# Performance work log

Measured on AMD Instinct MI355X. Metric: run time of the kernel, lower is better.

## Reference

```python
import jax, jax.numpy as jnp
import numpy as np
from jax.scipy.linalg import solve_triangular


def setup_inputs() -> dict:
    key = jax.random.key(0)
    k1, k2 = jax.random.split(key)
    # [K classes, N per class, D features] training embeddings
    src_seq = jax.random.normal(k1, (256, 64, 128), dtype=jnp.float32)
    # [M, D] vectors to project and pairwise-score (clustering inner loop)
    test = jax.random.normal(k2, (8192, 128), dtype=jnp.float32)
    return {"src_seq": src_seq, "test": test}


def _fit_model(src_seq):
    # Faithful port of compute_scatter_matrices + fit_model.
    # S_w, S_b are symmetric PSD, so solve(S_w,S_b) eig is replaced by the
    # equivalent (and differentiable) generalized symmetric eig via Cholesky
    # whitening; A_inverse and psi are invariant to eigvec scaling/order.
    K, N, D = src_seq.shape
    count = K * N
    mean_per_class = src_seq.mean(axis=1)            # [K, D]
    mean = src_seq.mean(axis=(0, 1))                 # [D]
    diff_w = src_seq - mean_per_class[:, None, :]    # [K, N, D]
    diff_b = mean_per_class - mean                   # [K, D]
    S_w = jnp.einsum('knd,kne->de', diff_w, diff_w) / count   # [D, D]
    S_b = (N * jnp.einsum('kd,ke->de', diff_b, diff_b)) / count

    L = jnp.linalg.cholesky(S_w)                     # S_w = L L^T
    # Msym = L^{-1} S_b L^{-T}
    tmp = solve_triangular(L, S_b, lower=True)
    Msym = solve_triangular(L, tmp.T, lower=True).T
    Msym = 0.5 * (Msym + Msym.T)
    evals, U = jnp.linalg.eigh(Msym)
    W = solve_triangular(L, U, lower=True, trans=1)  # W = L^{-T} U, eigvecs of S_w^{-1} S_b

    lambda_b = jnp.sum(W * (S_b @ W), axis=0)        # diag(W^T S_b W)
    lambda_w = jnp.sum(W * (S_w @ W), axis=0)        # diag(W^T S_w W)
    n = float(N)
    # A = W^{-T} diag(sqrt(n/(n-1) * lambda_w))  =>  A^{-1} = diag(1/sqrt(.)) W^T
    A_inverse = (1.0 / jnp.sqrt(n / (n - 1.0) * lambda_w))[:, None] * W.T
    psi = jnp.clip((n - 1.0) / n * (lambda_b / lambda_w) - 1.0 / n, 0.0)
    return A_inverse, mean, psi


def reference(src_seq, test):
    A_inverse, mean, psi = _fit_model(src_seq)
    # latent = A_inverse @ (x - mean), batched over rows
    latent = (test - mean) @ A_inverse.T             # [M, D]
    # Pairwise single-vector probability (calculate_probability_single),
    # vectorized over all (i, j) pairs, in log space:
    # log p(i,j) = -(v_i - v_j)^T diag(psi) (v_i - v_j)
    #             - 0.5 * (D*log(2*pi) + log(||psi||_F))
    D = latent.shape[1]
    q = jnp.sum(psi * latent * latent, axis=1)       # [M]
    G = (latent * psi) @ latent.T                    # [M, M]
    maha = q[:, None] + q[None, :] - 2.0 * G         # [M, M]
    log_div = 0.5 * (D * jnp.log(2.0 * jnp.pi) + jnp.log(jnp.linalg.norm(psi)))
    return -maha - log_div                           # [M, M] pairwise log-prob
```

## Files before the change

### kernel.cpp

```cpp
#include <hip/hip_runtime.h>
#include <math.h>


#define D 128
#define NCLS 256
#define NPC 64
#define MTEST 8192
#define COUNT (NCLS*NPC)

#define fMC    0
#define fMEAN  16384
#define fSCAL  16640
#define fMAT   32768
#define fSWRAW 442368
#define fPART  458752
#define fU     458752
#define fV     983040
#define fQ     1507328
#define fBBF   1515520

#define sP   0
#define sSB  1
#define sP2  2
#define sP3  3
#define sP4  4
#define sZ   5
#define sMm  7
#define sC2  8
#define sXH  10
#define sT2  11
#define sT3  12
#define sT4  13
#define sT8  14
#define sT12 15
#define sT16 16
#define sG0  18
#define sF   23

using short8 = __attribute__((ext_vector_type(8))) short;
using f32x4  = __attribute__((ext_vector_type(4))) float;

__device__ inline unsigned short f2bf(float f) {
  unsigned u = __float_as_uint(f);
  unsigned r = u + 0x7FFFu + ((u >> 16) & 1u);
  return (unsigned short)(r >> 16);
}
__device__ inline float bf2f(unsigned short h) {
  return __uint_as_float(((unsigned)h) << 16);
}
__device__ inline float valU(const unsigned short* m, int idx) {
  return bf2f(m[idx]) + bf2f(m[idx + 16384]);
}
__device__ inline void storeDual(unsigned short* m, int idx, float g) {
  unsigned short hb = f2bf(g);
  m[idx] = hb;
  m[16384 + idx] = f2bf(g - bf2f(hb));
}
__device__ inline unsigned short* MS(float* ws, int m) {
  return (unsigned short*)(ws + fMAT) + (size_t)m * 32768;
}
__device__ inline short8 st8(const unsigned short* L, int rloc, int colk) {
  unsigned u = ((unsigned)(rloc * 128 + colk)) ^ (((unsigned)(rloc & 7)) << 3);
  return *(const short8*)(L + u);
}
__device__ inline float stValU(const unsigned short* L, int rloc, int col) {
  unsigned u = ((unsigned)(rloc * 128 + col)) ^ (((unsigned)(rloc & 7)) << 3);
  return bf2f(L[u]) + bf2f(L[4096 + u]);
}
__device__ inline void stPutDual(unsigned short* L, int rloc, int col, float g) {
  unsigned u = ((unsigned)(rloc * 128 + col)) ^ (((unsigned)(rloc & 7)) << 3);
  unsigned short hb = f2bf(g);
  L[u] = hb;
  L[4096 + u] = f2bf(g - bf2f(hb));
}

__device__ __forceinline__ f32x4 tile_AB(const unsigned short* __restrict__ A, int rA,
                                         const unsigned short* __restrict__ B, int cB,
                                         int lane, f32x4 acc) {
  #pragma unroll
  for (int ks = 0; ks < 4; ks++) {
    int kb = ks * 32 + (lane >> 4) * 8;
    short8 ah = *(const short8*)(A + rA * 128 + kb);
    short8 al = *(const short8*)(A + 16384 + rA * 128 + kb);
    short8 bh = *(const short8*)(B + cB * 128 + kb);
    short8 bl = *(const short8*)(B + 16384 + cB * 128 + kb);
    acc = __builtin_amdgcn_mfma_f32_16x16x32_bf16(ah, bh, acc, 0, 0, 0);
    acc = __builtin_amdgcn_mfma_f32_16x16x32_bf16(al, bh, acc, 0, 0, 0);
    acc = __builtin_amdgcn_mfma_f32_16x16x32_bf16(ah, bl, acc, 0, 0, 0);
  }
  return acc;
}
__device__ __forceinline__ f32x4 tile_LB(const unsigned short* __restrict__ L, int rloc,
                                         const unsigned short* __restrict__ B, int cB,
                                         int lane, f32x4 acc) {
  #pragma unroll
  for (int ks = 0; ks < 4; ks++) {
    int kb = ks * 32 + (lane >> 4) * 8;
    short8 ah = st8(L, rloc, kb);
    short8 al = st8(L + 4096, rloc, kb);
    short8 bh = *(const short8*)(B + cB * 128 + kb);
    short8 bl = *(const short8*)(B + 16384 + cB * 128 + kb);
    acc = __builtin_amdgcn_mfma_f32_16x16x32_bf16(ah, bh, acc, 0, 0, 0);
    acc = __builtin_amdgcn_mfma_f32_16x16x32_bf16(al, bh, acc, 0, 0, 0);
    acc = __builtin_amdgcn_mfma_f32_16x16x32_bf16(ah, bl, acc, 0, 0, 0);
  }
  return acc;
}

__global__ __launch_bounds__(256) void k_gt_partial(const float* __restrict__ X, float* __restrict__ ws) {
  __shared__ unsigned short xt[128 * 256];
  int b = blockIdx.x, tid = threadIdx.x;
  const float* Xc = X + b * 256 * D;
  for (int idx = tid; idx < 256 * D; idx += 256) {
    int s = idx >> 7, d = idx & 127;
    unsigned byte = ((unsigned)(d * 512 + s * 2)) ^ (((unsigned)(d & 7)) << 4);
    *(unsigned short*)((char*)xt + byte) = f2bf(Xc[idx]);
  }
  {
    int d = tid & 127;
    for (int cc = (tid >> 7); cc < 4; cc += 2) {
      const float* p = Xc + cc * 64 * D + d;
      float s = 0.f;
      #pragma unroll
      for (int n = 0; n < 64; n++) s += p[n * D];
      ((unsigned short*)ws)[d * 256 + (b * 4 + cc)] = f2bf(s * (1.0f / 64.0f));
    }
  }
  __syncthreads();
  int w = tid >> 6, lane = tid & 63;
  int wr = (w >> 1) * 64, wc = (w & 1) * 64;
  f32x4 acc[4][4] = {};
  for (int ks = 0; ks < 8; ks++) {
    int kb = ks * 32 + (lane >> 4) * 8;
    short8 af[4];
    #pragma unroll
    for (int mt = 0; mt < 4; mt++) {
      int r = wr + mt * 16 + (lane & 15);
      unsigned byte = ((unsigned)(r * 512 + kb * 2)) ^ (((unsigned)(r & 7)) << 4);
      af[mt] = *(short8*)((char*)xt + byte);
    }
    #pragma unroll
    for (int nt = 0; nt < 4; nt++) {
      int c = wc + nt * 16 + (lane & 15);
      unsigned byte = ((unsigned)(c * 512 + kb * 2)) ^ (((unsigned)(c & 7)) << 4);
      short8 bfr = *(short8*)((char*)xt + byte);
      #pragma unroll
      for (int mt = 0; mt < 4; mt++)
        acc[mt][nt] = __builtin_amdgcn_mfma_f32_16x16x32_bf16(af[mt], bfr, acc[mt][nt], 0, 0, 0);
    }
  }
  float* outp = ws + fPART + b * 16384;
  #pragma unroll
  for (int mt = 0; mt < 4; mt++)
    #pragma unroll
    for (int nt = 0; nt < 4; nt++)
      #pragma unroll
      for (int r = 0; r < 4; r++) {
        int row = wr + mt * 16 + (lane >> 4) * 4 + r;
        int col = wc + nt * 16 + (lane & 15);
        outp[row * 128 + col] = acc[mt][nt][r];
      }
}

__global__ void k_reduce(float* __restrict__ ws) {
  __shared__ float red2[4];
  int tid = threadIdx.x;
  int idx = blockIdx.x * 256 + tid;
  const float* part = ws + fPART;
  float s = 0.f;
  #pragma unroll 8
  for (int p = 0; p < 64; p++) s += part[p * 16384 + idx];
  ws[fSWRAW + idx] = s;
  if (blockIdx.x == 0 && tid < 128) {
    const unsigned short* McT = (const unsigned short*)ws;
    float m = 0.f;
    for (int k = 0; k < 256; k++) m += bf2f(McT[tid * 256 + k]);
    ws[fMEAN + tid] = m * (1.0f / 256.0f);
  }
  if (blockIdx.x == 1) {
    float v = 0.f;
    if (tid < 128) {
      float gdd = 0.f;
      for (int p = 0; p < 64; p++) gdd += part[p * 16384 + tid * 129];
      const unsigned short* McT = (const unsigned short*)ws;
      float nrm = 0.f;
      for (int k = 0; k < 256; k++) { float x = bf2f(McT[tid * 256 + k]); nrm += x * x; }
      v = gdd * (1.0f / COUNT) - nrm * (1.0f / 256.0f);
    }
    #pragma unroll
    for (int off = 32; off > 0; off >>= 1) v += __shfl_down(v, off);
    if ((tid & 63) == 0) red2[tid >> 6] = v;
    __syncthreads();
    if (tid == 0) {
      float inv_s = 128.0f / (red2[0] + red2[1] + red2[2] + red2[3]);
      ws[fSCAL + 1] = inv_s;
      ws[fSCAL + 7] = 0.984375f * inv_s;
    }
  }
}

__global__ __launch_bounds__(1024) void k_sbp(float* __restrict__ ws) {
  const unsigned short* Mc = (const unsigned short*)ws;
  const float* mv = ws + fMEAN;
  const float* swraw = ws + fSWRAW;
  float inv_s = ws[fSCAL + 1];
  unsigned short* SB = MS(ws, sSB);
  unsigned short* P = MS(ws, sP);
  int tid = threadIdx.x, b = blockIdx.x;
  int w = tid >> 6, lane = tid & 63;
  int wr = (w & 1) * 16, wc = (w >> 1) * 16;
  int brow = b * 32;
  f32x4 acc = {};
  for (int ks = 0; ks < 8; ks++) {
    int kb = ks * 32 + (lane >> 4) * 8;
    short8 af = *(const short8*)(Mc + (brow + wr + (lane & 15)) * 256 + kb);
    short8 bf = *(const short8*)(Mc + (wc + (lane & 15)) * 256 + kb);
    acc = __builtin_amdgcn_mfma_f32_16x16x32_bf16(af, bf, acc, 0, 0, 0);
  }
  #pragma unroll
  for (int r = 0; r < 4; r++) {
    int row = brow + wr + (lane >> 4) * 4 + r;
    int col = wc + (lane & 15);
    int idx = row * 128 + col;
    float g = acc[r] * (1.0f / 256.0f) - mv[row] * mv[col];
    storeDual(SB, idx, g);
    float s = (swraw[idx] * (1.0f / COUNT) - g - mv[row] * mv[col]) * inv_s;
    storeDual(P, idx, s - ((row == col) ? 1.0f : 0.0f));
  }
}

__global__ __launch_bounds__(1024) void k_pows(const float* __restrict__ test, float* __restrict__ ws) {
  __shared__ unsigned short sA[8192];
  __shared__ unsigned short sB[8192];
  __shared__ float red[16];
  float* scal = ws + fSCAL;
  int tid = threadIdx.x, b = blockIdx.x;
  if (b >= 4) {
    unsigned short* Vbf = (unsigned short*)(ws + fV);
    const float* mv = ws + fMEAN;
    int base = (b - 4) * 32768;
    #pragma unroll 4
    for (int k = 0; k < 32; k++) {
      int idx = base + k * 1024 + tid;
      Vbf[idx] = f2bf(test[idx] - mv[idx & 127]);
    }
    return;
  }
  const unsigned short* P = MS(ws, sP);
  unsigned short* P2 = MS(ws, sP2);
  unsigned short* P3 = MS(ws, sP3);
  unsigned short* P4 = MS(ws, sP4);
  int w = tid >> 6, lane = tid & 63;
  int wr = (w & 1) * 16, wc = (w >> 1) * 16;
  int brow = b * 32;
  float tsum = 0.f;
  {
    f32x4 acc = {};
    acc = tile_AB(P, brow + wr + (lane & 15), P, wc + (lane & 15), lane, acc);
    #pragma unroll
    for (int r = 0; r < 4; r++) {
      int rloc = wr + (lane >> 4) * 4 + r;
      int col = wc + (lane & 15);
      float g = acc[r];
      stPutDual(sA, rloc, col, g);
      storeDual(P2, (brow + rloc) * 128 + col, g);
      tsum += g * g;
    }
  }
  #pragma unroll
  for (int off = 32; off > 0; off >>= 1) tsum += __shfl_down(tsum, off);
  if (lane == 0) red[w] = tsum;
  __syncthreads();
  if (tid == 0) {
    float s = 0.f;
    #pragma unroll
    for (int i = 0; i < 16; i++) s += red[i];
    scal[60 + b] = s;
  }
  {
    f32x4 acc = {};
    acc = tile_LB(sA, wr + (lane & 15), P, wc + (lane & 15), lane, acc);
    #pragma unroll
    for (int r = 0; r < 4; r++) {
      int rloc = wr + (lane >> 4) * 4 + r;
      int col = wc + (lane & 15);
      stPutDual(sB, rloc, col, acc[r]);
      storeDual(P3, (brow + rloc) * 128 + col, acc[r]);
    }
  }
  __syncthreads();
  {
    f32x4 acc = {};
    acc = tile_LB(sB, wr + (lane & 15), P, wc + (lane & 15), lane, acc);
    #pragma unroll
    for (int r = 0; r < 4; r++) {
      int rloc = wr + (lane >> 4) * 4 + r;
      int col = wc + (lane & 15);
      storeDual(P4, (brow + rloc) * 128 + col, acc[r]);
    }
  }
}

__global__ __launch_bounds__(256) void k_z(float* __restrict__ ws) {
  __shared__ float cj[5];
  __shared__ float bt[5];
  float* scal = ws + fSCAL;
  int tid = threadIdx.x;
  float trP4 = scal[60] + scal[61] + scal[62] + scal[63];
  float a = 1.05f * sqrtf(sqrtf(fmaxf(trP4, 1e-30f)));
  a = fminf(fmaxf(a, 1e-3f), 0.95f);
  if (tid < 5) {
    const float PI = 3.14159265358979f;
    float s = 0.f;
    for (int i = 0; i < 64; i++) {
      float th = (i + 0.5f) * (PI / 64.0f);
      float x = cosf(th);
      s += (1.0f / sqrtf(1.0f + a * x)) * cosf((float)tid * th);
    }
    cj[tid] = s * (2.0f / 64.0f);
  }
  __syncthreads();
  if (tid == 0) {
    float c0h = 0.5f * cj[0];
    float m0 = c0h - cj[2] + cj[4];
    float m1 = cj[1] - 3.0f * cj[3];
    float m2 = 2.0f * cj[2] - 8.0f * cj[4];
    float m3 = 4.0f * cj[3];
    float m4 = 8.0f * cj[4];
    float ia = 1.0f / a, p = 1.f;
    bt[0] = m0;
    p *= ia; bt[1] = m1 * p;
    p *= ia; bt[2] = m2 * p;
    p *= ia; bt[3] = m3 * p;
    p *= ia; bt[4] = m4 * p;
  }
  __syncthreads();
  const unsigned short *P = MS(ws, sP), *P2 = MS(ws, sP2),
    *P3 = MS(ws, sP3), *P4 = MS(ws, sP4);
  unsigned short* Z = MS(ws, sZ);
  float b0 = bt[0], b1 = bt[1], b2 = bt[2], b3 = bt[3], b4 = bt[4];
  int gid = blockIdx.x * 256 + tid;
  #pragma unroll
  for (int t = 0; t < 4; t++) {
    int idx = gid * 4 + t;
    int row = idx >> 7, col = idx & 127;
    float dg = (row == col) ? 1.0f : 0.0f;
    float z = b0 * dg + b1 * valU(P, idx) + b2 * valU(P2, idx) +
              b3 * valU(P3, idx) + b4 * valU(P4, idx);
    storeDual(Z, idx, z);
  }
}

__global__ __launch_bounds__(1024) void k_m(float* __restrict__ ws) {
  __shared__ unsigned short sA[8192];
  const unsigned short* Z = MS(ws, sZ);
  const unsigned short* SB = MS(ws, sSB);
  unsigned short* Mm = MS(ws, sMm);
  int tid = threadIdx.x, b = blockIdx.x;
  int w = tid >> 6, lane = tid & 63;
  int wr = (w & 1) * 16, wc = (w >> 1) * 16;
  int brow = b * 32;
  {
    f32x4 acc = {};
    acc = tile_AB(Z, brow + wr + (lane & 15), SB, wc + (lane & 15), lane, acc);
    #pragma unroll
    for (int r = 0; r < 4; r++)
      stPutDual(sA, wr + (lane >> 4) * 4 + r, wc + (lane & 15), acc[r]);
  }
  __syncthreads();
  {
    f32x4 acc = {};
    acc = tile_LB(sA, wr + (lane & 15), Z, wc + (lane & 15), lane, acc);
    #pragma unroll
    for (int r = 0; r < 4; r++) {
      int rloc = wr + (lane >> 4) * 4 + r;
      storeDual(Mm, (brow + rloc) * 128 + wc + (lane & 15), acc[r]);
    }
  }
}

__global__ __launch_bounds__(1024) void k_c2(float* __restrict__ ws) {
  __shared__ float red[16];
  float* scal = ws + fSCAL;
  const unsigned short* Mm = MS(ws, sMm);
  unsigned short* C2 = MS(ws, sC2);
  int tid = threadIdx.x, b = blockIdx.x;
  int w = tid >> 6, lane = tid & 63;
  int wr = (w & 1) * 16, wc = (w >> 1) * 16;
  int brow = b * 32;
  f32x4 acc = {};
  acc = tile_AB(Mm, brow + wr + (lane & 15), Mm, wc + (lane & 15), lane, acc);
  float tsum = 0.f;
  #pragma unroll
  for (int r = 0; r < 4; r++) {
    int rloc = wr + (lane >> 4) * 4 + r;
    float g = acc[r];
    storeDual(C2, (brow + rloc) * 128 + wc + (lane & 15), g);
    tsum += g * g;
  }
  #pragma unroll
  for (int off = 32; off > 0; off >>= 1) tsum += __shfl_down(tsum, off);
  if (lane == 0) red[w] = tsum;
  __syncthreads();
  if (tid == 0) {
    float s = 0.f;
    #pragma unroll
    for (int i = 0; i < 16; i++) s += red[i];
    scal[68 + b] = s;
  }
}

__device__ inline void interval_cs(const float* scal, float* c0o, float* iho) {
  float trM4 = scal[68] + scal[69] + scal[70] + scal[71];
  float Lam = 1.03f * sqrtf(sqrtf(fmaxf(trM4, 1e-37f)));
  float lo = -0.02f * Lam, hi = Lam;
  *c0o = 0.5f * (hi + lo);
  *iho = 1.0f / (0.5f * (hi - lo));
}

__global__ __launch_bounds__(256) void k_xh_t2(float* __restrict__ ws) {
  __shared__ float cs[2];
  float* scal = ws + fSCAL;
  if (threadIdx.x == 0) {
    float c0, ih;
    interval_cs(scal, &c0, &ih);
    cs[0] = c0; cs[1] = ih;
  }
  __syncthreads();
  float c0 = cs[0], ih = cs[1];
  float a2 = 2.0f * ih * ih, b2 = -4.0f * c0 * ih * ih, g2 = 2.0f * c0 * c0 * ih * ih - 1.0f;
  const unsigned short* Mm = MS(ws, sMm);
  const unsigned short* C2 = MS(ws, sC2);
  unsigned short* XH = MS(ws, sXH);
  unsigned short* T2 = MS(ws, sT2);
  int gid = blockIdx.x * 256 + threadIdx.x;
  #pragma unroll
  for (int t = 0; t < 4; t++) {
    int idx = gid * 4 + t;
    int row = idx >> 7, col = idx & 127;
    float m = valU(Mm, idx), c2v = valU(C2, idx);
    float dg = (row == col) ? 1.0f : 0.0f;
    storeDual(XH, idx, ih * m - ih * c0 * dg);
    storeDual(T2, idx, a2 * c2v + b2 * m + g2 * dg);
  }
}

__global__ __launch_bounds__(1024) void k_t34(float* __restrict__ ws) {
  const unsigned short* XH = MS(ws, sXH);
  const unsigned short* T2 = MS(ws, sT2);
  int tid = threadIdx.x;
  int w = tid >> 6, lane = tid & 63;
  int wr = (w & 1) * 16, wc = (w >> 1) * 16;
  if (blockIdx.x < 4) {
    int brow = blockIdx.x * 32;
    f32x4 acc = {};
    acc = tile_AB(XH, brow + wr + (lane & 15), T2, wc + (lane & 15), lane, acc);
    unsigned short* T3 = MS(ws, sT3);
    #pragma unroll
    for (int r = 0; r < 4; r++) {
      int idx = (brow + wr + (lane >> 4) * 4 + r) * 128 + wc + (lane & 15);
      storeDual(T3, idx, 2.0f * acc[r] - valU(XH, idx));
    }
  } else {
    int brow = (blockIdx.x - 4) * 32;
    f32x4 acc = {};
    acc = tile_AB(T2, brow + wr + (lane & 15), T2, wc + (lane & 15), lane, acc);
    unsigned short* T4 = MS(ws, sT4);
    #pragma unroll
    for (int r = 0; r < 4; r++) {
      int row = brow + wr + (lane >> 4) * 4 + r;
      int col = wc + (lane & 15);
      storeDual(T4, row * 128 + col, 2.0f * acc[r] - ((row == col) ? 1.0f : 0.0f));
    }
  }
}

__global__ __launch_bounds__(1024) void k_t8g(float* __restrict__ ws) {
  __shared__ unsigned short sA[8192];
  __shared__ unsigned short sB[8192];
  __shared__ float cs[4];
  __shared__ float sat[20];
  __shared__ float sc[20];
  float* scal = ws + fSCAL;
  int tid = threadIdx.x;
  const unsigned short* T4 = MS(ws, sT4);
  if (blockIdx.x < 4) {
    int b = blockIdx.x, brow = b * 32;
    int w = tid >> 6, lane = tid & 63;
    int wr = (w & 1) * 16, wc = (w >> 1) * 16;
    unsigned short* T8 = MS(ws, sT8);
    unsigned short* T12 = MS(ws, sT12);
    unsigned short* T16 = MS(ws, sT16);
    {
      f32x4 acc = {};
      acc = tile_AB(T4, brow + wr + (lane & 15), T4, wc + (lane & 15), lane, acc);
      #pragma unroll
      for (int r = 0; r < 4; r++) {
        int rloc = wr + (lane >> 4) * 4 + r;
        int row = brow + rloc, col = wc + (lane & 15);
        float g = 2.0f * acc[r] - ((row == col) ? 1.0f : 0.0f);
        stPutDual(sA, rloc, col, g);
        storeDual(T8, row * 128 + col, g);
      }
    }
    __syncthreads();
    {
      f32x4 acc = {};
      acc = tile_LB(sA, wr + (lane & 15), T4, wc + (lane & 15), lane, acc);
      #pragma unroll
      for (int r = 0; r < 4; r++) {
        int rloc = wr + (lane >> 4) * 4 + r;
        int col = wc + (lane & 15);
        int idx = (brow + rloc) * 128 + col;
        float g = 2.0f * acc[r] - valU(T4, idx);
        stPutDual(sB, rloc, col, g);
        storeDual(T12, idx, g);
      }
    }
    __syncthreads();
    {
      f32x4 acc = {};
      acc = tile_LB(sB, wr + (lane & 15), T4, wc + (lane & 15), lane, acc);
      #pragma unroll
      for (int r = 0; r < 4; r++) {
        int rloc = wr + (lane >> 4) * 4 + r;
        int col = wc + (lane & 15);
        float g = 2.0f * acc[r] - stValU(sA, rloc, col);
        storeDual(T16, (brow + rloc) * 128 + col, g);
      }
    }
    return;
  }
  if (tid == 0) {
    float c0, ih;
    interval_cs(scal, &c0, &ih);
    float inv_s = scal[1];
    float t0 = (1.0f / 63.0f) / inv_s;
    float x0 = fminf(fmaxf((t0 - c0) * ih, -1.0f), 1.0f);
    cs[0] = acosf(x0); cs[1] = x0;
    cs[2] = 0.984375f * inv_s / ih;
  }
  __syncthreads();
  if (tid <= 19) {
    float th = cs[0], x0 = cs[1], SCc = cs[2];
    const float PI = 3.14159265358979f;
    float v;
    if (tid == 0) v = 0.5f * SCc * (2.0f / PI) * (sinf(th) - x0 * th);
    else if (tid == 1) v = SCc * (2.0f / PI) * (0.5f * th + 0.25f * sinf(2.0f * th) - x0 * sinf(th));
    else {
      float fj = (float)tid;
      v = SCc * (2.0f / PI) *
          (0.5f * (sinf((fj + 1.0f) * th) / (fj + 1.0f) + sinf((fj - 1.0f) * th) / (fj - 1.0f))
           - x0 * sinf(fj * th) / fj);
    }
    sat[tid] = v;
    sc[tid] = 0.f;
  }
  __syncthreads();
  if (tid == 0) {
    for (int j = 19; j >= 4; --j) {
      int k = j >> 2, r = j & 3;
      float aj = sat[j];
      if (r == 0) sc[k * 4] += aj;
      else { sc[k * 4 + r] += 2.0f * aj; sat[4 * k - r] -= aj; }
    }
    for (int r = 0; r < 4; r++) sc[r] += sat[r];
  }
  __syncthreads();
  const unsigned short* XH = MS(ws, sXH);
  const unsigned short* T2 = MS(ws, sT2);
  const unsigned short* T3 = MS(ws, sT3);
  int idx = (blockIdx.x - 4) * 1024 + tid;
  {
    int row = idx >> 7, col = idx & 127;
    float dg = (row == col) ? 1.0f : 0.0f;
    float x1 = valU(XH, idx), x2 = valU(T2, idx), x3 = valU(T3, idx);
    #pragma unroll
    for (int k = 0; k < 5; k++) {
      float g = sc[k * 4 + 0] * dg + sc[k * 4 + 1] * x1 + sc[k * 4 + 2] * x2 +
                sc[k * 4 + 3] * x3;
      storeDual(MS(ws, sG0 + k), idx, g);
    }
  }
}

__global__ __launch_bounds__(1024) void k_bigF(float* __restrict__ ws) {
  __shared__ float red[16];
  float* scal = ws + fSCAL;
  const unsigned short* G0 = MS(ws, sG0);
  unsigned short* Fm = MS(ws, sF);
  int tid = threadIdx.x, b = blockIdx.x;
  int w = tid >> 6, lane = tid & 63;
  int wr = (w & 1) * 16, wc = (w >> 1) * 16;
  int brow = b * 32;
  int rA = brow + wr + (lane & 15), cB = wc + (lane & 15);
  f32x4 acc = {};
  acc = tile_AB(MS(ws, sT4), rA, MS(ws, sG0 + 1), cB, lane, acc);
  acc = tile_AB(MS(ws, sT8), rA, MS(ws, sG0 + 2), cB, lane, acc);
  acc = tile_AB(MS(ws, sT12), rA, MS(ws, sG0 + 3), cB, lane, acc);
  acc = tile_AB(MS(ws, sT16), rA, MS(ws, sG0 + 4), cB, lane, acc);
  float tsum = 0.f;
  #pragma unroll
  for (int r = 0; r < 4; r++) {
    int rloc = wr + (lane >> 4) * 4 + r;
    int idx = (brow + rloc) * 128 + wc + (lane & 15);
    float g = acc[r] + valU(G0, idx);
    storeDual(Fm, idx, g);
    tsum += g * g;
  }
  #pragma unroll
  for (int off = 32; off > 0; off >>= 1) tsum += __shfl_down(tsum, off);
  if (lane == 0) red[w] = tsum;
  __syncthreads();
  if (tid == 0) {
    float s = 0.f;
    #pragma unroll
    for (int i = 0; i < 16; i++) s += red[i];
    scal[72 + b] = s;
  }
}

__global__ __launch_bounds__(1024) void k_b(float* __restrict__ ws) {
  __shared__ unsigned short sA[8192];
  const unsigned short* Z = MS(ws, sZ);
  const unsigned short* Fm = MS(ws, sF);
  unsigned short* Bbf = (unsigned short*)(ws + fBBF);
  float aeff = ws[fSCAL + 7];
  int tid = threadIdx.x, b = blockIdx.x;
  int w = tid >> 6, lane = tid & 63;
  int wr = (w & 1) * 16, wc = (w >> 1) * 16;
  int brow = b * 32;
  {
    f32x4 acc = {};
    acc = tile_AB(Z, brow + wr + (lane & 15), Fm, wc + (lane & 15), lane, acc);
    #pragma unroll
    for (int r = 0; r < 4; r++)
      stPutDual(sA, wr + (lane >> 4) * 4 + r, wc + (lane & 15), acc[r]);
  }
  __syncthreads();
  {
    f32x4 acc = {};
    acc = tile_LB(sA, wr + (lane & 15), Z, wc + (lane & 15), lane, acc);
    #pragma unroll
    for (int r = 0; r < 4; r++) {
      int rloc = wr + (lane >> 4) * 4 + r;
      Bbf[(brow + rloc) * 128 + wc + (lane & 15)] = f2bf(acc[r] * aeff);
    }
  }
}

__global__ __launch_bounds__(256) void k_latent(float* __restrict__ ws) {
  __shared__ unsigned short vh[16384];
  __shared__ float qs[128];
  int blk = blockIdx.x, tid = threadIdx.x;
  if (blk == 0 && tid == 0) {
    float* scal = ws + fSCAL;
    float trF2 = fmaxf(scal[72] + scal[73] + scal[74] + scal[75], 1e-30f);
    scal[0] = 0.5f * (128.0f * 1.8378770664093453f + 0.5f * logf(trF2));
  }
  const unsigned short* Vbf = (const unsigned short*)(ws + fV);
  if (tid < 128) qs[tid] = 0.f;
  for (int idx = tid; idx < 16384; idx += 256) {
    int r = idx >> 7, c = idx & 127;
    unsigned short h = Vbf[blk * 16384 + idx];
    unsigned byte = ((unsigned)(r * 256 + c * 2)) ^ (((unsigned)(r & 7)) << 4);
    *(unsigned short*)((char*)vh + byte) = h;
  }
  __syncthreads();
  int w = tid >> 6, lane = tid & 63;
  int wr = (w >> 1) * 64, wc = (w & 1) * 64;
  const unsigned short* Bbf = (const unsigned short*)(ws + fBBF);
  f32x4 acc[4][4] = {};
  for (int ks = 0; ks < 4; ks++) {
    int kb = ks * 32 + (lane >> 4) * 8;
    short8 af[4], bfv[4];
    #pragma unroll
    for (int mt = 0; mt < 4; mt++) {
      int r = wr + mt * 16 + (lane & 15);
      unsigned byte = ((unsigned)(r * 256 + kb * 2)) ^ (((unsigned)(r & 7)) << 4);
      af[mt] = *(short8*)((char*)vh + byte);
    }
    #pragma unroll
    for (int nt = 0; nt < 4; nt++) {
      int c = wc + nt * 16 + (lane & 15);
      bfv[nt] = *(const short8*)(Bbf + c * 128 + kb);
    }
    #pragma unroll
    for (int mt = 0; mt < 4; mt++)
      #pragma unroll
      for (int nt = 0; nt < 4; nt++)
        acc[mt][nt] = __builtin_amdgcn_mfma_f32_16x16x32_bf16(af[mt], bfv[nt], acc[mt][nt], 0, 0, 0);
  }
  unsigned short* Ubf = (unsigned short*)(ws + fU);
  #pragma unroll
  for (int mt = 0; mt < 4; mt++)
    #pragma unroll
    for (int nt = 0; nt < 4; nt++)
      #pragma unroll
      for (int r = 0; r < 4; r++) {
        int row = wr + mt * 16 + (lane >> 4) * 4 + r;
        int col = wc + nt * 16 + (lane & 15);
        Ubf[(blk * 128 + row) * 128 + col] = f2bf(acc[mt][nt][r]);
      }
  #pragma unroll
  for (int mt = 0; mt < 4; mt++)
    #pragma unroll
    for (int r = 0; r < 4; r++) {
      int row = wr + mt * 16 + (lane >> 4) * 4 + r;
      float p = 0.f;
      #pragma unroll
      for (int nt = 0; nt < 4; nt++) {
        int col = wc + nt * 16 + (lane & 15);
        unsigned byte = ((unsigned)(row * 256 + col * 2)) ^ (((unsigned)(row & 7)) << 4);
        p += bf2f(f2bf(acc[mt][nt][r])) * bf2f(*(unsigned short*)((char*)vh + byte));
      }
      p += __shfl_xor(p, 1, 16);
      p += __shfl_xor(p, 2, 16);
      p += __shfl_xor(p, 4, 16);
      p += __shfl_xor(p, 8, 16);
      if ((lane & 15) == 0) atomicAdd(&qs[row], p);
    }
  __syncthreads();
  if (tid < 128) ws[fQ + blk * 128 + tid] = qs[tid];
}

__global__ __launch_bounds__(256) void k_pair(const float* __restrict__ ws, float* __restrict__ out) {
  __shared__ float qi[128];
  __shared__ float qj[128];
  __shared__ float sld;
  int bi = blockIdx.x, bj = blockIdx.y, tid = threadIdx.x;
  if (tid < 128) qi[tid] = ws[fQ + bi * 128 + tid];
  else qj[tid - 128] = ws[fQ + bj * 128 + (tid - 128)];
  if (tid == 0) sld = ws[fSCAL + 0];
  __syncthreads();
  int w = tid >> 6, lane = tid & 63;
  int wr = (w >> 1) * 64, wc = (w & 1) * 64;
  const unsigned short* Ubf = (const unsigned short*)(ws + fU);
  const unsigned short* Vbf = (const unsigned short*)(ws + fV);
  f32x4 acc[4][4] = {};
  for (int ks = 0; ks < 4; ks++) {
    int kb = ks * 32 + (lane >> 4) * 8;
    short8 af[4], bfv[4];
    #pragma unroll
    for (int mt = 0; mt < 4; mt++) {
      int r = bi * 128 + wr + mt * 16 + (lane & 15);
      af[mt] = *(const short8*)(Ubf + r * 128 + kb);
    }
    #pragma unroll
    for (int nt = 0; nt < 4; nt++) {
      int c = bj * 128 + wc + nt * 16 + (lane & 15);
      bfv[nt] = *(const short8*)(Vbf + c * 128 + kb);
    }
    #pragma unroll
    for (int mt = 0; mt < 4; mt++)
      #pragma unroll
      for (int nt = 0; nt < 4; nt++)
        acc[mt][nt] = __builtin_amdgcn_mfma_f32_16x16x32_bf16(af[mt], bfv[nt], acc[mt][nt], 0, 0, 0);
  }
  float ld = sld;
  #pragma unroll
  for (int mt = 0; mt < 4; mt++)
    #pragma unroll
    for (int nt = 0; nt < 4; nt++)
      #pragma unroll
      for (int r = 0; r < 4; r++) {
        int row = wr + mt * 16 + (lane >> 4) * 4 + r;
        int col = wc + nt * 16 + (lane & 15);
        float g = acc[mt][nt][r];
        out[(size_t)(bi * 128 + row) * MTEST + (bj * 128 + col)] =
          2.0f * g - qi[row] - qj[col] - ld;
      }
}

extern "C" void kernel_launch(void* const* d_in, const int* in_sizes, int n_in,
                              void* d_out, int out_size, void* d_ws, size_t ws_size,
                              hipStream_t stream) {
  (void)in_sizes; (void)n_in; (void)out_size; (void)ws_size;
  const float* X = (const float*)d_in[0];
  const float* test = (const float*)d_in[1];
  float* out = (float*)d_out;
  float* ws = (float*)d_ws;

  k_gt_partial<<<64, 256, 0, stream>>>(X, ws);
  k_reduce<<<64, 256, 0, stream>>>(ws);
  k_sbp<<<4, 1024, 0, stream>>>(ws);
  k_pows<<<36, 1024, 0, stream>>>(test, ws);
  k_z<<<16, 256, 0, stream>>>(ws);
  k_m<<<4, 1024, 0, stream>>>(ws);
  k_c2<<<4, 1024, 0, stream>>>(ws);
  k_xh_t2<<<16, 256, 0, stream>>>(ws);
  k_t34<<<8, 1024, 0, stream>>>(ws);
  k_t8g<<<20, 1024, 0, stream>>>(ws);
  k_bigF<<<4, 1024, 0, stream>>>(ws);
  k_b<<<4, 1024, 0, stream>>>(ws);
  k_latent<<<64, 256, 0, stream>>>(ws);
  k_pair<<<dim3(64, 64), 256, 0, stream>>>(ws, out);
}
```

Before: 271.3 us.

## Fuse Z build into M kernel and XH/T2 build into T34; nontemporal output stores

Merges k_z with k_m and k_xh_t2 with k_t34. Each block recomputes the full elementwise matrix (Z or T2) into shared memory using a swizzled layout, so the following GEMMs read operands from LDS instead of global memory. This removes two kernel launches and their global round-trips on the serial small-matrix chain, but every block now redundantly recomputes the whole 128x128 matrix and uses about 80KB of LDS. Separately, the large pairwise output write now uses nontemporal stores to avoid polluting the cache.

```diff
diff --git a/kernel.cpp b/kernel.cpp
--- a/kernel.cpp
+++ b/kernel.cpp
@@ -73,6 +73,16 @@
   L[u] = hb;
   L[4096 + u] = f2bf(g - bf2f(hb));
 }
+__device__ inline short8 lf8(const unsigned short* L, int row, int colk) {
+  unsigned u = ((unsigned)(row * 128 + colk)) ^ (((unsigned)(row & 7)) << 3);
+  return *(const short8*)(L + u);
+}
+__device__ inline void lfPutDual(unsigned short* L, int row, int col, float g) {
+  unsigned u = ((unsigned)(row * 128 + col)) ^ (((unsigned)(row & 7)) << 3);
+  unsigned short hb = f2bf(g);
+  L[u] = hb;
+  L[16384 + u] = f2bf(g - bf2f(hb));
+}
 
 __device__ __forceinline__ f32x4 tile_AB(const unsigned short* __restrict__ A, int rA,
                                          const unsigned short* __restrict__ B, int cB,
@@ -100,6 +110,53 @@
     short8 al = st8(L + 4096, rloc, kb);
     short8 bh = *(const short8*)(B + cB * 128 + kb);
     short8 bl = *(const short8*)(B + 16384 + cB * 128 + kb);
+    acc = __builtin_amdgcn_mfma_f32_16x16x32_bf16(ah, bh, acc, 0, 0, 0);
+    acc = __builtin_amdgcn_mfma_f32_16x16x32_bf16(al, bh, acc, 0, 0, 0);
+    acc = __builtin_amdgcn_mfma_f32_16x16x32_bf16(ah, bl, acc, 0, 0, 0);
+  }
+  return acc;
+}
+__device__ __forceinline__ f32x4 tile_FG(const unsigned short* __restrict__ Lf, int rA,
+                                         const unsigned short* __restrict__ B, int cB,
+                                         int lane, f32x4 acc) {
+  #pragma unroll
+  for (int ks = 0; ks < 4; ks++) {
+    int kb = ks * 32 + (lane >> 4) * 8;
+    short8 ah = lf8(Lf, rA, kb);
+    short8 al = lf8(Lf + 16384, rA, kb);
+    short8 bh = *(const short8*)(B + cB * 128 + kb);
+    short8 bl = *(const short8*)(B + 16384 + cB * 128 + kb);
+    acc = __builtin_amdgcn_mfma_f32_16x16x32_bf16(ah, bh, acc, 0, 0, 0);
+    acc = __builtin_amdgcn_mfma_f32_16x16x32_bf16(al, bh, acc, 0, 0, 0);
+    acc = __builtin_amdgcn_mfma_f32_16x16x32_bf16(ah, bl, acc, 0, 0, 0);
+  }
+  return acc;
+}
+__device__ __forceinline__ f32x4 tile_SF(const unsigned short* __restrict__ Ls, int rloc,
+                                         const unsigned short* __restrict__ Lf, int cB,
+                                         int lane, f32x4 acc) {
+  #pragma unroll
+  for (int ks = 0; ks < 4; ks++) {
+    int kb = ks * 32 + (lane >> 4) * 8;
+    short8 ah = st8(Ls, rloc, kb);
+    short8 al = st8(Ls + 4096, rloc, kb);
+    short8 bh = lf8(Lf, cB, kb);
+    short8 bl = lf8(Lf + 16384, cB, kb);
+    acc = __builtin_amdgcn_mfma_f32_16x16x32_bf16(ah, bh, acc, 0, 0, 0);
+    acc = __builtin_amdgcn_mfma_f32_16x16x32_bf16(al, bh, acc, 0, 0, 0);
+    acc = __builtin_amdgcn_mfma_f32_16x16x32_bf16(ah, bl, acc, 0, 0, 0);
+  }
+  return acc;
+}
+__device__ __forceinline__ f32x4 tile_FF(const unsigned short* __restrict__ Lf, int rA,
+                                         int cB, int lane, f32x4 acc) {
+  #pragma unroll
+  for (int ks = 0; ks < 4; ks++) {
+    int kb = ks * 32 + (lane >> 4) * 8;
+    short8 ah = lf8(Lf, rA, kb);
+    short8 al = lf8(Lf + 16384, rA, kb);
+    short8 bh = lf8(Lf, cB, kb);
+    short8 bl = lf8(Lf + 16384, cB, kb);
     acc = __builtin_amdgcn_mfma_f32_16x16x32_bf16(ah, bh, acc, 0, 0, 0);
     acc = __builtin_amdgcn_mfma_f32_16x16x32_bf16(al, bh, acc, 0, 0, 0);
     acc = __builtin_amdgcn_mfma_f32_16x16x32_bf16(ah, bl, acc, 0, 0, 0);
@@ -301,11 +358,13 @@
   }
 }
 
-__global__ __launch_bounds__(256) void k_z(float* __restrict__ ws) {
+__global__ __launch_bounds__(1024) void k_zm(float* __restrict__ ws) {
+  __shared__ unsigned short shZ[32768];
+  __shared__ unsigned short shA[8192];
   __shared__ float cj[5];
   __shared__ float bt[5];
   float* scal = ws + fSCAL;
-  int tid = threadIdx.x;
+  int tid = threadIdx.x, b = blockIdx.x;
   float trP4 = scal[60] + scal[61] + scal[62] + scal[63];
   float a = 1.05f * sqrtf(sqrtf(fmaxf(trP4, 1e-30f)));
   a = fminf(fmaxf(a, 1e-3f), 0.95f);
@@ -337,40 +396,33 @@
   __syncthreads();
   const unsigned short *P = MS(ws, sP), *P2 = MS(ws, sP2),
     *P3 = MS(ws, sP3), *P4 = MS(ws, sP4);
-  unsigned short* Z = MS(ws, sZ);
+  unsigned short* Zg = MS(ws, sZ);
   float b0 = bt[0], b1 = bt[1], b2 = bt[2], b3 = bt[3], b4 = bt[4];
-  int gid = blockIdx.x * 256 + tid;
-  #pragma unroll
-  for (int t = 0; t < 4; t++) {
-    int idx = gid * 4 + t;
+  for (int idx = tid; idx < 16384; idx += 1024) {
     int row = idx >> 7, col = idx & 127;
     float dg = (row == col) ? 1.0f : 0.0f;
     float z = b0 * dg + b1 * valU(P, idx) + b2 * valU(P2, idx) +
               b3 * valU(P3, idx) + b4 * valU(P4, idx);
-    storeDual(Z, idx, z);
-  }
-}
-
-__global__ __launch_bounds__(1024) void k_m(float* __restrict__ ws) {
-  __shared__ unsigned short sA[8192];
-  const unsigned short* Z = MS(ws, sZ);
+    lfPutDual(shZ, row, col, z);
+    if ((row >> 5) == b) storeDual(Zg, idx, z);
+  }
+  __syncthreads();
   const unsigned short* SB = MS(ws, sSB);
   unsigned short* Mm = MS(ws, sMm);
-  int tid = threadIdx.x, b = blockIdx.x;
   int w = tid >> 6, lane = tid & 63;
   int wr = (w & 1) * 16, wc = (w >> 1) * 16;
   int brow = b * 32;
   {
     f32x4 acc = {};
-    acc = tile_AB(Z, brow + wr + (lane & 15), SB, wc + (lane & 15), lane, acc);
+    acc = tile_FG(shZ, brow + wr + (lane & 15), SB, wc + (lane & 15), lane, acc);
     #pragma unroll
     for (int r = 0; r < 4; r++)
-      stPutDual(sA, wr + (lane >> 4) * 4 + r, wc + (lane & 15), acc[r]);
+      stPutDual(shA, wr + (lane >> 4) * 4 + r, wc + (lane & 15), acc[r]);
   }
   __syncthreads();
   {
     f32x4 acc = {};
-    acc = tile_LB(sA, wr + (lane & 15), Z, wc + (lane & 15), lane, acc);
+    acc = tile_SF(shA, wr + (lane & 15), shZ, wc + (lane & 15), lane, acc);
     #pragma unroll
     for (int r = 0; r < 4; r++) {
       int rloc = wr + (lane >> 4) * 4 + r;
@@ -418,53 +470,62 @@
   *iho = 1.0f / (0.5f * (hi - lo));
 }
 
-__global__ __launch_bounds__(256) void k_xh_t2(float* __restrict__ ws) {
+__global__ __launch_bounds__(1024) void k_t34(float* __restrict__ ws) {
+  __shared__ unsigned short shT2[32768];
+  __shared__ unsigned short shXH[8192];
   __shared__ float cs[2];
   float* scal = ws + fSCAL;
-  if (threadIdx.x == 0) {
+  int tid = threadIdx.x, b = blockIdx.x;
+  if (tid == 0) {
     float c0, ih;
     interval_cs(scal, &c0, &ih);
     cs[0] = c0; cs[1] = ih;
   }
   __syncthreads();
   float c0 = cs[0], ih = cs[1];
-  float a2 = 2.0f * ih * ih, b2 = -4.0f * c0 * ih * ih, g2 = 2.0f * c0 * c0 * ih * ih - 1.0f;
+  float a2 = 2.0f * ih * ih, b2c = -4.0f * c0 * ih * ih, g2 = 2.0f * c0 * c0 * ih * ih - 1.0f;
   const unsigned short* Mm = MS(ws, sMm);
   const unsigned short* C2 = MS(ws, sC2);
-  unsigned short* XH = MS(ws, sXH);
-  unsigned short* T2 = MS(ws, sT2);
-  int gid = blockIdx.x * 256 + threadIdx.x;
-  #pragma unroll
-  for (int t = 0; t < 4; t++) {
-    int idx = gid * 4 + t;
+  unsigned short* T2g = MS(ws, sT2);
+  unsigned short* XHg = MS(ws, sXH);
+  bool isT3 = (b < 4);
+  int bs = isT3 ? b : (b - 4);
+  int brow = bs * 32;
+  for (int idx = tid; idx < 16384; idx += 1024) {
     int row = idx >> 7, col = idx & 127;
     float m = valU(Mm, idx), c2v = valU(C2, idx);
     float dg = (row == col) ? 1.0f : 0.0f;
-    storeDual(XH, idx, ih * m - ih * c0 * dg);
-    storeDual(T2, idx, a2 * c2v + b2 * m + g2 * dg);
-  }
-}
-
-__global__ __launch_bounds__(1024) void k_t34(float* __restrict__ ws) {
-  const unsigned short* XH = MS(ws, sXH);
-  const unsigned short* T2 = MS(ws, sT2);
-  int tid = threadIdx.x;
+    float t2 = a2 * c2v + b2c * m + g2 * dg;
+    lfPutDual(shT2, row, col, t2);
+    if (!isT3 && (row >> 5) == bs) storeDual(T2g, idx, t2);
+  }
+  if (isT3) {
+    for (int idx = tid; idx < 4096; idx += 1024) {
+      int rloc = idx >> 7, col = idx & 127;
+      int row = brow + rloc;
+      int gidx = row * 128 + col;
+      float m = valU(Mm, gidx);
+      float xh = ih * m - ih * c0 * ((row == col) ? 1.0f : 0.0f);
+      stPutDual(shXH, rloc, col, xh);
+      storeDual(XHg, gidx, xh);
+    }
+  }
+  __syncthreads();
   int w = tid >> 6, lane = tid & 63;
   int wr = (w & 1) * 16, wc = (w >> 1) * 16;
-  if (blockIdx.x < 4) {
-    int brow = blockIdx.x * 32;
+  if (isT3) {
     f32x4 acc = {};
-    acc = tile_AB(XH, brow + wr + (lane & 15), T2, wc + (lane & 15), lane, acc);
+    acc = tile_SF(shXH, wr + (lane & 15), shT2, wc + (lane & 15), lane, acc);
     unsigned short* T3 = MS(ws, sT3);
     #pragma unroll
     for (int r = 0; r < 4; r++) {
-      int idx = (brow + wr + (lane >> 4) * 4 + r) * 128 + wc + (lane & 15);
-      storeDual(T3, idx, 2.0f * acc[r] - valU(XH, idx));
+      int rloc = wr + (lane >> 4) * 4 + r;
+      int col = wc + (lane & 15);
+      storeDual(T3, (brow + rloc) * 128 + col, 2.0f * acc[r] - stValU(shXH, rloc, col));
     }
   } else {
-    int brow = (blockIdx.x - 4) * 32;
     f32x4 acc = {};
-    acc = tile_AB(T2, brow + wr + (lane & 15), T2, wc + (lane & 15), lane, acc);
+    acc = tile_FF(shT2, brow + wr + (lane & 15), wc + (lane & 15), lane, acc);
     unsigned short* T4 = MS(ws, sT4);
     #pragma unroll
     for (int r = 0; r < 4; r++) {
@@ -767,8 +828,9 @@
         int row = wr + mt * 16 + (lane >> 4) * 4 + r;
         int col = wc + nt * 16 + (lane & 15);
         float g = acc[mt][nt][r];
-        out[(size_t)(bi * 128 + row) * MTEST + (bj * 128 + col)] =
-          2.0f * g - qi[row] - qj[col] - ld;
+        float v = 2.0f * g - qi[row] - qj[col] - ld;
+        __builtin_nontemporal_store(v,
+          &out[(size_t)(bi * 128 + row) * MTEST + (bj * 128 + col)]);
       }
 }
 
@@ -785,10 +847,8 @@
   k_reduce<<<64, 256, 0, stream>>>(ws);
   k_sbp<<<4, 1024, 0, stream>>>(ws);
   k_pows<<<36, 1024, 0, stream>>>(test, ws);
-  k_z<<<16, 256, 0, stream>>>(ws);
-  k_m<<<4, 1024, 0, stream>>>(ws);
+  k_zm<<<4, 1024, 0, stream>>>(ws);
   k_c2<<<4, 1024, 0, stream>>>(ws);
-  k_xh_t2<<<16, 256, 0, stream>>>(ws);
   k_t34<<<8, 1024, 0, stream>>>(ws);
   k_t8g<<<20, 1024, 0, stream>>>(ws);
   k_bigF<<<4, 1024, 0, stream>>>(ws);
```

Measured after the change: 283.5 us. +4.5%, slower.
